# Kernel optimization log

Measured on AMD Instinct MI355X. Metric: run time of the kernel, lower is better.

The kernel has to match this reference:

```python
import jax, jax.numpy as jnp
import numpy as np
from jax import lax

BATCH = 4096
HID = 512
T = 20


def setup_inputs() -> dict:
    key = jax.random.key(0)
    ks = jax.random.split(key, 12)
    B2 = BATCH * 2
    inp = {
        "x": jax.random.normal(ks[0], (BATCH, 2, T, 2), jnp.float32),
        "x_agents": jax.random.normal(ks[1], (BATCH, 2), jnp.float32),  # unused by forward
        "h0": jax.random.normal(ks[2], (B2, HID), jnp.float32),
        "c0": jax.random.normal(ks[3], (B2, HID), jnp.float32),
        # LSTMCell params (PyTorch layout: gates stacked as [i, f, g, o])
        "W_ih": jax.random.normal(ks[4], (4 * HID, 2), jnp.float32) * 0.05,
        "W_hh": jax.random.normal(ks[5], (4 * HID, HID), jnp.float32) * 0.05,
        "b_ih": jax.random.normal(ks[6], (4 * HID,), jnp.float32) * 0.05,
        "b_hh": jax.random.normal(ks[7], (4 * HID,), jnp.float32) * 0.05,
        # MLP head
        "fc1_w": jax.random.normal(ks[8], (HID, 2 * T * HID), jnp.float32) * 0.01,
        "fc1_b": jax.random.normal(ks[9], (HID,), jnp.float32) * 0.01,
        "fc2_w": jax.random.normal(ks[10], (1, HID), jnp.float32) * 0.05,
        "fc2_b": jax.random.normal(ks[11], (1,), jnp.float32) * 0.05,
        "training_step": 2,
    }
    return inp


def reference(x, x_agents, h0, c0, W_ih, W_hh, b_ih, b_hh, fc1_w, fc1_b, fc2_w, fc2_b, training_step):
    # training_step == 2 path (default) of the original module.
    batch = x.shape[0]
    H = W_hh.shape[1]
    xs = x.reshape(batch * 2, T, 2).transpose(1, 0, 2)  # [T, B2, 2]

    def step(carry, xt):
        h, c = carry
        gates = xt @ W_ih.T + b_ih + h @ W_hh.T + b_hh  # [B2, 4H]
        i, f, g, o = jnp.split(gates, 4, axis=-1)
        i = jax.nn.sigmoid(i)
        f = jax.nn.sigmoid(f)
        g = jnp.tanh(g)
        o = jax.nn.sigmoid(o)
        c_new = f * c + i * g
        h_new = o * jnp.tanh(c_new)
        return (h_new, c_new), h_new

    _, hs = lax.scan(step, (h0, c0), xs)  # hs: [T, B2, H]
    states = hs.transpose(1, 0, 2).reshape(batch, 2 * T * H)  # [batch, 2*T*H]
    out = jax.nn.relu(states @ fc1_w.T + fc1_b) @ fc2_w.T + fc2_b
    return jax.nn.sigmoid(out)
```

## Files before the change

kernel.cpp:

```cpp
#include <hip/hip_runtime.h>
#include <hip/hip_bf16.h>

#define TSTEPS 20
#define SMEM_BYTES 131072

typedef __bf16 bf16x8 __attribute__((ext_vector_type(8)));
typedef float f32x4 __attribute__((ext_vector_type(4)));
typedef unsigned short u16;

__device__ __forceinline__ u16 f2bf(float f) {
  unsigned u = __builtin_bit_cast(unsigned, f);
  u = (u + 0x7FFFu + ((u >> 16) & 1u)) >> 16;
  return (u16)u;
}
__device__ __forceinline__ float rcp_(float v) { return __builtin_amdgcn_rcpf(v); }
__device__ __forceinline__ float sig_(float v) { return rcp_(1.f + __expf(-v)); }
__device__ __forceinline__ float tanh_(float v) { return 1.f - 2.f * rcp_(1.f + __expf(2.f * v)); }

#define MFMA16(a, b, c) __builtin_amdgcn_mfma_f32_16x16x32_bf16((a), (b), (c), 0, 0, 0)
#define BAR() asm volatile("s_barrier" ::: "memory")
#define WAITV(n) asm volatile("s_waitcnt vmcnt(" #n ")" ::: "memory")
#define WAITLG() asm volatile("s_waitcnt lgkmcnt(0)" ::: "memory")

__device__ __forceinline__ void gload16(const u16* g, u16* lds) {
#if defined(__HIP_DEVICE_COMPILE__)
  __builtin_amdgcn_global_load_lds(
      (const __attribute__((address_space(1))) unsigned*)g,
      (__attribute__((address_space(3))) unsigned*)lds, 16, 0, 0);
#endif
}

__global__ void convert_f32_bf16(const float* __restrict__ s, u16* __restrict__ d, int n) {
  int i = (blockIdx.x * blockDim.x + threadIdx.x) * 4;
  if (i + 3 < n) {
    float4 v = *reinterpret_cast<const float4*>(s + i);
    ushort4 o;
    o.x = f2bf(v.x); o.y = f2bf(v.y); o.z = f2bf(v.z); o.w = f2bf(v.w);
    *reinterpret_cast<ushort4*>(d + i) = o;
  }
}

__global__ void convert_whh_p(const float* __restrict__ w, u16* __restrict__ d) {
  int p = blockIdx.x;
  int k = threadIdx.x;
  int j = p & 15, f = (p >> 4) & 3, wg = (p >> 6) & 3, s = p >> 8;
  int orig = (f << 9) + (s << 6) + (wg << 4) + j;
  d[p * 512 + k] = f2bf(w[orig * 512 + k]);
}

__global__ void bx_prep(const float* __restrict__ Wih, const float* __restrict__ bih,
                        const float* __restrict__ bhh, u16* __restrict__ Bx) {
  int p = blockIdx.x * blockDim.x + threadIdx.x;
  if (p >= 2048) return;
  int j = p & 15, f = (p >> 4) & 3, wg = (p >> 6) & 3, s = p >> 8;
  int o = (f << 9) + (s << 6) + (wg << 4) + j;
  u16* row = Bx + p * 32;
  row[0] = f2bf(Wih[o * 2 + 0]);
  row[1] = f2bf(Wih[o * 2 + 1]);
  row[2] = f2bf(bih[o] + bhh[o]);
#pragma unroll
  for (int k = 3; k < 32; ++k) row[k] = 0;
}

__global__ void init_state(const float* __restrict__ h0, const float* __restrict__ c0,
                           u16* __restrict__ hbf, float* __restrict__ cws,
                           float* __restrict__ facc, int nh, int nacc) {
  int i = blockIdx.x * blockDim.x + threadIdx.x;
  if (i < nh) {
    hbf[i] = f2bf(h0[i]);
    int r = i & 3, mt = (i >> 2) & 7, lane = (i >> 5) & 63, wid = (i >> 11) & 7, bid = i >> 14;
    int s = (bid >> 3) & 7, nb = (bid & 7) * 4 + (bid >> 6);
    int wm = wid >> 2, wn = wid & 3;
    int jl = lane & 15, kg = lane >> 4;
    int n = nb * 256 + wm * 128 + mt * 16 + kg * 4 + r;
    int u = s * 64 + wn * 16 + jl;
    cws[i] = c0[n * 512 + u];
  }
  if (i < nacc) facc[i] = 0.f;
}

__global__ __launch_bounds__(512, 1) void step256(
    const u16* __restrict__ Wp,
    const u16* __restrict__ Bxg,
    const float* __restrict__ x,
    const u16* __restrict__ hin,
    u16* __restrict__ hout,
    float* __restrict__ cws,
    const u16* __restrict__ fc1w,
    float* __restrict__ facc,
    int t, int doLstm, int doFc1) {
  extern __shared__ char S[];

  const int tid = threadIdx.x;
  const int lane = tid & 63, wid = tid >> 6;
  const int jl = lane & 15, kg = lane >> 4;
  const int bid = blockIdx.x;
  const int s = (bid >> 3) & 7;
  const int nb = (bid & 7) * 4 + (bid >> 6);
  const int n0 = nb * 256;
  const int srow = tid >> 3;
  const int sw = (tid & 7) ^ (srow & 7);

  if (doLstm) {
    const int wm = wid >> 2, wn = wid & 3;
    const int u = s * 64 + wn * 16 + jl;
    const int swz0 = (kg ^ (jl & 7)) * 16;
    const int swz1 = ((4 + kg) ^ (jl & 7)) * 16;
    const int aB0 = wm * 16384 + jl * 128 + swz0;
    const int aB1 = wm * 16384 + jl * 128 + swz1;
    const int bB0 = 32768 + wn * 8192 + jl * 128 + swz0;
    const int bB1 = 32768 + wn * 8192 + jl * 128 + swz1;
    const u16* srcA = hin + (n0 + srow) * 512 + sw * 8;
    const u16* srcB = Wp + (s * 256 + srow) * 512 + sw * 8;

    f32x4 acc[8][4];
#pragma unroll
    for (int mt = 0; mt < 8; ++mt)
#pragma unroll
      for (int f = 0; f < 4; ++f) acc[mt][f] = (f32x4){0.f, 0.f, 0.f, 0.f};

    float2 xv = {0.f, 0.f};
    if (tid < 256) xv = *reinterpret_cast<const float2*>(x + (n0 + tid) * 40 + t * 2);
    {
      const int r0 = tid >> 2, ch = tid & 3;
      gload16(Bxg + (s * 256 + 0 * 128 + r0) * 32 + ch * 8, (u16*)(S + 32768 + 0 * 8192 + wid * 1024));
      gload16(Bxg + (s * 256 + 1 * 128 + r0) * 32 + ch * 8, (u16*)(S + 32768 + 1 * 8192 + wid * 1024));
    }
#pragma unroll
    for (int q = 0; q < 4; ++q) {
      gload16(srcA + q * 32768, (u16*)(S + 65536 + q * 8192 + wid * 1024));
      gload16(srcB + q * 32768, (u16*)(S + 65536 + 32768 + q * 8192 + wid * 1024));
    }
    if (tid < 256) {
      u16 row0[8] = {f2bf(xv.x), f2bf(xv.y), 0x3F80u, 0, 0, 0, 0, 0};
      *reinterpret_cast<uint4*>(S + tid * 64) = *reinterpret_cast<const uint4*>(row0);
      uint4 z = {0u, 0u, 0u, 0u};
      *reinterpret_cast<uint4*>(S + tid * 64 + 16) = z;
      *reinterpret_cast<uint4*>(S + tid * 64 + 32) = z;
      *reinterpret_cast<uint4*>(S + tid * 64 + 48) = z;
    }
    WAITLG();
    WAITV(8);
    BAR();
    {
#pragma unroll
      for (int mt = 0; mt < 8; ++mt) {
        bf16x8 a = *reinterpret_cast<const bf16x8*>(S + (wm * 128 + mt * 16 + jl) * 64 + kg * 16);
#pragma unroll
        for (int f = 0; f < 4; ++f) {
          bf16x8 b = *reinterpret_cast<const bf16x8*>(S + 32768 + (wn * 64 + f * 16 + jl) * 64 + kg * 16);
          acc[mt][f] = MFMA16(a, b, acc[mt][f]);
        }
      }
    }
    BAR();

#define LSTAGE(kt, p)                                                              \
  do {                                                                             \
    _Pragma("unroll") for (int q = 0; q < 4; ++q) {                                \
      gload16(srcA + q * 32768 + (kt) * 64, (u16*)(S + (p) * 65536 + q * 8192 + wid * 1024)); \
      gload16(srcB + q * 32768 + (kt) * 64, (u16*)(S + (p) * 65536 + 32768 + q * 8192 + wid * 1024)); \
    }                                                                              \
  } while (0)
#define LCOMP(p)                                                                   \
  do {                                                                             \
    bf16x8 a0[8], b0[4];                                                           \
    _Pragma("unroll") for (int mt = 0; mt < 8; ++mt)                               \
        a0[mt] = *reinterpret_cast<const bf16x8*>(S + (p) * 65536 + aB0 + mt * 2048); \
    _Pragma("unroll") for (int f = 0; f < 4; ++f)                                  \
        b0[f] = *reinterpret_cast<const bf16x8*>(S + (p) * 65536 + bB0 + f * 2048); \
    _Pragma("unroll") for (int mt = 0; mt < 8; ++mt)                               \
      _Pragma("unroll") for (int f = 0; f < 4; ++f)                                \
        acc[mt][f] = MFMA16(a0[mt], b0[f], acc[mt][f]);                            \
    _Pragma("unroll") for (int mt = 0; mt < 8; ++mt)                               \
        a0[mt] = *reinterpret_cast<const bf16x8*>(S + (p) * 65536 + aB1 + mt * 2048); \
    _Pragma("unroll") for (int f = 0; f < 4; ++f)                                  \
        b0[f] = *reinterpret_cast<const bf16x8*>(S + (p) * 65536 + bB1 + f * 2048); \
    _Pragma("unroll") for (int mt = 0; mt < 8; ++mt)                               \
      _Pragma("unroll") for (int f = 0; f < 4; ++f)                                \
        acc[mt][f] = MFMA16(a0[mt], b0[f], acc[mt][f]);                            \
  } while (0)

#pragma unroll
    for (int kt = 0; kt < 8; ++kt) {
      if (kt < 7) {
        if ((kt + 1) & 1) LSTAGE(kt + 1, 0); else LSTAGE(kt + 1, 1);
        WAITV(8);
      } else {
        WAITV(0);
      }
      BAR();
      if (kt & 1) LCOMP(0); else LCOMP(1);
      BAR();
    }

    float* cbase = cws + ((bid * 8 + wid) * 64 + lane) * 32;
#pragma unroll
    for (int mt = 0; mt < 8; ++mt) {
      f32x4 cv = *reinterpret_cast<f32x4*>(cbase + mt * 4);
      f32x4 cn;
      float hn[4];
#pragma unroll
      for (int r = 0; r < 4; ++r) {
        float iv = sig_(acc[mt][0][r]);
        float fv = sig_(acc[mt][1][r]);
        float gv = tanh_(acc[mt][2][r]);
        float ov = sig_(acc[mt][3][r]);
        float c2 = fv * cv[r] + iv * gv;
        cn[r] = c2;
        hn[r] = ov * tanh_(c2);
      }
      *reinterpret_cast<f32x4*>(cbase + mt * 4) = cn;
#pragma unroll
      for (int r = 0; r < 4; ++r)
        hout[(n0 + wm * 128 + mt * 16 + kg * 4 + r) * 512 + u] = f2bf(hn[r]);
    }
  }

  if (doFc1) {
    const int Fm0 = nb * 128, Fj0 = s * 64;
    const int Fwm = wid >> 1, Fwn = wid & 1;
    const int tf = t - 1;
    const int swz0 = (kg ^ (jl & 7)) * 16;
    const int swz1 = ((4 + kg) ^ (jl & 7)) * 16;
    const int faB0 = Fwm * 4096 + jl * 128 + swz0;
    const int faB1 = Fwm * 4096 + jl * 128 + swz1;
    const int fbB0 = 16384 + Fwn * 4096 + jl * 128 + swz0;
    const int fbB1 = 16384 + Fwn * 4096 + jl * 128 + swz1;
    const u16* fsrcA = hin + 2 * (Fm0 + srow) * 512 + sw * 8;
    const u16* fsrcB = fc1w + (Fj0 + srow) * 20480 + tf * 512 + sw * 8;

    f32x4 fa[2][2];
#pragma unroll
    for (int a = 0; a < 2; ++a)
#pragma unroll
      for (int b = 0; b < 2; ++b) fa[a][b] = (f32x4){0.f, 0.f, 0.f, 0.f};

#define FSTAGE(kt, p)                                                              \
  do {                                                                             \
    const int an_ = (kt) >> 3, kc_ = ((kt) & 7) * 64;                              \
    gload16(fsrcA + 0 * 65536 + an_ * 512 + kc_, (u16*)(S + (p) * 32768 + 0 * 8192 + wid * 1024)); \
    gload16(fsrcA + 1 * 65536 + an_ * 512 + kc_, (u16*)(S + (p) * 32768 + 1 * 8192 + wid * 1024)); \
    gload16(fsrcB + an_ * 10240 + kc_, (u16*)(S + (p) * 32768 + 16384 + wid * 1024)); \
  } while (0)
#define FCOMP(p)                                                                   \
  do {                                                                             \
    bf16x8 af[2], bf[2];                                                           \
    _Pragma("unroll") for (int mf = 0; mf < 2; ++mf)                               \
        af[mf] = *reinterpret_cast<const bf16x8*>(S + (p) * 32768 + faB0 + mf * 2048); \
    _Pragma("unroll") for (int jf = 0; jf < 2; ++jf)                               \
        bf[jf] = *reinterpret_cast<const bf16x8*>(S + (p) * 32768 + fbB0 + jf * 2048); \
    _Pragma("unroll") for (int mf = 0; mf < 2; ++mf)                               \
      _Pragma("unroll") for (int jf = 0; jf < 2; ++jf)                             \
        fa[mf][jf] = MFMA16(af[mf], bf[jf], fa[mf][jf]);                           \
    _Pragma("unroll") for (int mf = 0; mf < 2; ++mf)                               \
        af[mf] = *reinterpret_cast<const bf16x8*>(S + (p) * 32768 + faB1 + mf * 2048); \
    _Pragma("unroll") for (int jf = 0; jf < 2; ++jf)                               \
        bf[jf] = *reinterpret_cast<const bf16x8*>(S + (p) * 32768 + fbB1 + jf * 2048); \
    _Pragma("unroll") for (int mf = 0; mf < 2; ++mf)                               \
      _Pragma("unroll") for (int jf = 0; jf < 2; ++jf)                             \
        fa[mf][jf] = MFMA16(af[mf], bf[jf], fa[mf][jf]);                           \
  } while (0)

    FSTAGE(0, 0);
#pragma unroll
    for (int kt = 0; kt < 16; ++kt) {
      if (kt < 15) {
        if ((kt + 1) & 1) FSTAGE(kt + 1, 1); else FSTAGE(kt + 1, 0);
        WAITV(3);
      } else {
        WAITV(0);
      }
      BAR();
      if (kt & 1) FCOMP(1); else FCOMP(0);
      BAR();
    }
#pragma unroll
    for (int mf = 0; mf < 2; ++mf)
#pragma unroll
      for (int jf = 0; jf < 2; ++jf) {
        int j = Fj0 + Fwn * 32 + jf * 16 + jl;
#pragma unroll
        for (int r = 0; r < 4; ++r) {
          int m = Fm0 + Fwm * 32 + mf * 16 + kg * 4 + r;
          facc[m * 512 + j] += fa[mf][jf][r];
        }
      }
  }
}

__global__ __launch_bounds__(256) void head_kernel(
    const float* __restrict__ acc, const float* __restrict__ fc1b,
    const float* __restrict__ fc2w, const float* __restrict__ fc2b,
    float* __restrict__ out) {
  int lane = threadIdx.x & 63;
  int row = blockIdx.x * 4 + (threadIdx.x >> 6);
  float sum = 0.f;
#pragma unroll
  for (int j = lane; j < 512; j += 64)
    sum += fmaxf(acc[row * 512 + j] + fc1b[j], 0.f) * fc2w[j];
#pragma unroll
  for (int off = 32; off; off >>= 1) sum += __shfl_down(sum, off);
  if (lane == 0) out[row] = sig_(sum + fc2b[0]);
}

extern "C" void kernel_launch(void* const* d_in, const int* in_sizes, int n_in,
                              void* d_out, int out_size, void* d_ws, size_t ws_size,
                              hipStream_t stream) {
  const float* x = (const float*)d_in[0];
  const float* h0 = (const float*)d_in[2];
  const float* c0 = (const float*)d_in[3];
  const float* Wih = (const float*)d_in[4];
  const float* Whh = (const float*)d_in[5];
  const float* bih = (const float*)d_in[6];
  const float* bhh = (const float*)d_in[7];
  const float* fc1w = (const float*)d_in[8];
  const float* fc1b = (const float*)d_in[9];
  const float* fc2w = (const float*)d_in[10];
  const float* fc2b = (const float*)d_in[11];
  float* out = (float*)d_out;

  char* ws = (char*)d_ws;
  const size_t MB = 1 << 20;
  u16* Wp = (u16*)(ws);
  u16* fc1_bf = (u16*)(ws + 2 * MB);
  u16* hbf0 = (u16*)(ws + 22 * MB);
  u16* hbf1 = (u16*)(ws + 30 * MB);
  float* cws = (float*)(ws + 38 * MB);
  float* facc = (float*)(ws + 54 * MB);
  u16* Bxg = (u16*)(ws + 62 * MB);

  (void)hipFuncSetAttribute(reinterpret_cast<const void*>(step256),
                            hipFuncAttributeMaxDynamicSharedMemorySize, SMEM_BYTES);

  convert_whh_p<<<2048, 512, 0, stream>>>(Whh, Wp);
  bx_prep<<<8, 256, 0, stream>>>(Wih, bih, bhh, Bxg);
  convert_f32_bf16<<<10240, 256, 0, stream>>>(fc1w, fc1_bf, 512 * 20480);
  init_state<<<16384, 256, 0, stream>>>(h0, c0, hbf0, cws, facc, 8192 * 512, 4096 * 512);

  u16* hb[2] = {hbf0, hbf1};
  for (int t = 0; t <= TSTEPS; ++t) {
    step256<<<256, 512, SMEM_BYTES, stream>>>(
        Wp, Bxg, x, hb[t & 1], hb[(t + 1) & 1], cws, fc1_bf, facc,
        t, t < TSTEPS ? 1 : 0, t > 0 ? 1 : 0);
  }
  head_kernel<<<1024, 256, 0, stream>>>(facc, fc1b, fc2w, fc2b, out);
}
```

Before: 712.2 us.

## Fuse fc1 accumulation into LSTM K-loop reusing staged h tiles from LDS

The fc1 partial GEMM for the previous timestep now runs inside the LSTM recurrent K-loop. It reads the h tile already staged in LDS instead of loading h and fc1 weights through a separate pipelined phase. fc1 weights are pre-permuted into an MFMA-fragment layout so each lane loads its B operands directly from global memory, and a small fc1_tail kernel handles the final timestep. This removes the second load pipeline and extra barriers per step, at the cost of more register pressure and global loads interleaved with the LSTM MFMAs, plus s_setprio hints.

```diff
diff --git a/kernel.cpp b/kernel.cpp
--- a/kernel.cpp
+++ b/kernel.cpp
@@ -30,22 +30,30 @@
 #endif
 }
 
-__global__ void convert_f32_bf16(const float* __restrict__ s, u16* __restrict__ d, int n) {
-  int i = (blockIdx.x * blockDim.x + threadIdx.x) * 4;
-  if (i + 3 < n) {
-    float4 v = *reinterpret_cast<const float4*>(s + i);
-    ushort4 o;
-    o.x = f2bf(v.x); o.y = f2bf(v.y); o.z = f2bf(v.z); o.w = f2bf(v.w);
-    *reinterpret_cast<ushort4*>(d + i) = o;
-  }
-}
-
 __global__ void convert_whh_p(const float* __restrict__ w, u16* __restrict__ d) {
   int p = blockIdx.x;
   int k = threadIdx.x;
   int j = p & 15, f = (p >> 4) & 3, wg = (p >> 6) & 3, s = p >> 8;
   int orig = (f << 9) + (s << 6) + (wg << 4) + j;
   d[p * 512 + k] = f2bf(w[orig * 512 + k]);
+}
+
+__global__ void fc1p_prep(const float* __restrict__ w, u16* __restrict__ d) {
+  int id = blockIdx.x * blockDim.x + threadIdx.x;
+  int jl = id & 15, t1 = id >> 4;
+  int kg = t1 & 3, t2 = t1 >> 2;
+  int jf = t2 & 1, t3 = t2 >> 1;
+  int Fwn = t3 & 1, t4 = t3 >> 1;
+  int kk2 = t4 & 31, t5 = t4 >> 5;
+  int tf = t5 % 20, s = t5 / 20;
+  int j = s * 64 + Fwn * 32 + jf * 16 + jl;
+  int k = kk2 * 32 + kg * 8;
+  const float* src = w + j * 20480 + (k >> 9) * 10240 + tf * 512 + (k & 511);
+  float4 v0 = *reinterpret_cast<const float4*>(src);
+  float4 v1 = *reinterpret_cast<const float4*>(src + 4);
+  u16* dst = d + id * 8;
+  dst[0] = f2bf(v0.x); dst[1] = f2bf(v0.y); dst[2] = f2bf(v0.z); dst[3] = f2bf(v0.w);
+  dst[4] = f2bf(v1.x); dst[5] = f2bf(v1.y); dst[6] = f2bf(v1.z); dst[7] = f2bf(v1.w);
 }
 
 __global__ void bx_prep(const float* __restrict__ Wih, const float* __restrict__ bih,
@@ -86,9 +94,9 @@
     const u16* __restrict__ hin,
     u16* __restrict__ hout,
     float* __restrict__ cws,
-    const u16* __restrict__ fc1w,
+    const u16* __restrict__ fc1p,
     float* __restrict__ facc,
-    int t, int doLstm, int doFc1) {
+    int t, int doFacc) {
   extern __shared__ char S[];
 
   const int tid = threadIdx.x;
@@ -101,59 +109,66 @@
   const int srow = tid >> 3;
   const int sw = (tid & 7) ^ (srow & 7);
 
-  if (doLstm) {
-    const int wm = wid >> 2, wn = wid & 3;
-    const int u = s * 64 + wn * 16 + jl;
-    const int swz0 = (kg ^ (jl & 7)) * 16;
-    const int swz1 = ((4 + kg) ^ (jl & 7)) * 16;
-    const int aB0 = wm * 16384 + jl * 128 + swz0;
-    const int aB1 = wm * 16384 + jl * 128 + swz1;
-    const int bB0 = 32768 + wn * 8192 + jl * 128 + swz0;
-    const int bB1 = 32768 + wn * 8192 + jl * 128 + swz1;
-    const u16* srcA = hin + (n0 + srow) * 512 + sw * 8;
-    const u16* srcB = Wp + (s * 256 + srow) * 512 + sw * 8;
-
-    f32x4 acc[8][4];
-#pragma unroll
-    for (int mt = 0; mt < 8; ++mt)
-#pragma unroll
-      for (int f = 0; f < 4; ++f) acc[mt][f] = (f32x4){0.f, 0.f, 0.f, 0.f};
-
-    float2 xv = {0.f, 0.f};
-    if (tid < 256) xv = *reinterpret_cast<const float2*>(x + (n0 + tid) * 40 + t * 2);
-    {
-      const int r0 = tid >> 2, ch = tid & 3;
-      gload16(Bxg + (s * 256 + 0 * 128 + r0) * 32 + ch * 8, (u16*)(S + 32768 + 0 * 8192 + wid * 1024));
-      gload16(Bxg + (s * 256 + 1 * 128 + r0) * 32 + ch * 8, (u16*)(S + 32768 + 1 * 8192 + wid * 1024));
-    }
-#pragma unroll
-    for (int q = 0; q < 4; ++q) {
-      gload16(srcA + q * 32768, (u16*)(S + 65536 + q * 8192 + wid * 1024));
-      gload16(srcB + q * 32768, (u16*)(S + 65536 + 32768 + q * 8192 + wid * 1024));
-    }
-    if (tid < 256) {
-      u16 row0[8] = {f2bf(xv.x), f2bf(xv.y), 0x3F80u, 0, 0, 0, 0, 0};
-      *reinterpret_cast<uint4*>(S + tid * 64) = *reinterpret_cast<const uint4*>(row0);
-      uint4 z = {0u, 0u, 0u, 0u};
-      *reinterpret_cast<uint4*>(S + tid * 64 + 16) = z;
-      *reinterpret_cast<uint4*>(S + tid * 64 + 32) = z;
-      *reinterpret_cast<uint4*>(S + tid * 64 + 48) = z;
-    }
-    WAITLG();
-    WAITV(8);
-    BAR();
-    {
-#pragma unroll
-      for (int mt = 0; mt < 8; ++mt) {
-        bf16x8 a = *reinterpret_cast<const bf16x8*>(S + (wm * 128 + mt * 16 + jl) * 64 + kg * 16);
-#pragma unroll
-        for (int f = 0; f < 4; ++f) {
-          bf16x8 b = *reinterpret_cast<const bf16x8*>(S + 32768 + (wn * 64 + f * 16 + jl) * 64 + kg * 16);
-          acc[mt][f] = MFMA16(a, b, acc[mt][f]);
-        }
-      }
-    }
-    BAR();
+  const int wm = wid >> 2, wn = wid & 3;
+  const int Fwm = wid >> 1, Fwn = wid & 1;
+  const int u = s * 64 + wn * 16 + jl;
+  const int tf = (t > 0) ? (t - 1) : 0;
+  const int swz0 = (kg ^ (jl & 7)) * 16;
+  const int swz1 = ((4 + kg) ^ (jl & 7)) * 16;
+  const int aB0 = wm * 16384 + jl * 128 + swz0;
+  const int aB1 = wm * 16384 + jl * 128 + swz1;
+  const int bB0 = 32768 + wn * 8192 + jl * 128 + swz0;
+  const int bB1 = 32768 + wn * 8192 + jl * 128 + swz1;
+  const u16* srcA = hin + (n0 + srow) * 512 + sw * 8;
+  const u16* srcB = Wp + (s * 256 + srow) * 512 + sw * 8;
+  const u16* fbl = fc1p + (s * 20 + tf) * 65536 + Fwn * 1024 + kg * 128 + jl * 8;
+
+  f32x4 acc[8][4];
+#pragma unroll
+  for (int mt = 0; mt < 8; ++mt)
+#pragma unroll
+    for (int f = 0; f < 4; ++f) acc[mt][f] = (f32x4){0.f, 0.f, 0.f, 0.f};
+  f32x4 fa[2][2];
+#pragma unroll
+  for (int a = 0; a < 2; ++a)
+#pragma unroll
+    for (int b = 0; b < 2; ++b) fa[a][b] = (f32x4){0.f, 0.f, 0.f, 0.f};
+
+  float2 xv = {0.f, 0.f};
+  if (tid < 256) xv = *reinterpret_cast<const float2*>(x + (n0 + tid) * 40 + t * 2);
+  {
+    const int r0 = tid >> 2, ch = tid & 3;
+    gload16(Bxg + (s * 256 + 0 * 128 + r0) * 32 + ch * 8, (u16*)(S + 32768 + 0 * 8192 + wid * 1024));
+    gload16(Bxg + (s * 256 + 1 * 128 + r0) * 32 + ch * 8, (u16*)(S + 32768 + 1 * 8192 + wid * 1024));
+  }
+#pragma unroll
+  for (int q = 0; q < 4; ++q) {
+    gload16(srcA + q * 32768, (u16*)(S + 65536 + q * 8192 + wid * 1024));
+    gload16(srcB + q * 32768, (u16*)(S + 65536 + 32768 + q * 8192 + wid * 1024));
+  }
+  if (tid < 256) {
+    u16 row0[8] = {f2bf(xv.x), f2bf(xv.y), 0x3F80u, 0, 0, 0, 0, 0};
+    *reinterpret_cast<uint4*>(S + tid * 64) = *reinterpret_cast<const uint4*>(row0);
+    uint4 z = {0u, 0u, 0u, 0u};
+    *reinterpret_cast<uint4*>(S + tid * 64 + 16) = z;
+    *reinterpret_cast<uint4*>(S + tid * 64 + 32) = z;
+    *reinterpret_cast<uint4*>(S + tid * 64 + 48) = z;
+  }
+  WAITLG();
+  WAITV(8);
+  BAR();
+  {
+#pragma unroll
+    for (int mt = 0; mt < 8; ++mt) {
+      bf16x8 a = *reinterpret_cast<const bf16x8*>(S + (wm * 128 + mt * 16 + jl) * 64 + kg * 16);
+#pragma unroll
+      for (int f = 0; f < 4; ++f) {
+        bf16x8 b = *reinterpret_cast<const bf16x8*>(S + 32768 + (wn * 64 + f * 16 + jl) * 64 + kg * 16);
+        acc[mt][f] = MFMA16(a, b, acc[mt][f]);
+      }
+    }
+  }
+  BAR();
 
 #define LSTAGE(kt, p)                                                              \
   do {                                                                             \
@@ -182,99 +197,71 @@
   } while (0)
 
 #pragma unroll
-    for (int kt = 0; kt < 8; ++kt) {
-      if (kt < 7) {
-        if ((kt + 1) & 1) LSTAGE(kt + 1, 0); else LSTAGE(kt + 1, 1);
-        WAITV(8);
-      } else {
-        WAITV(0);
-      }
-      BAR();
-      if (kt & 1) LCOMP(0); else LCOMP(1);
-      BAR();
-    }
-
-    float* cbase = cws + ((bid * 8 + wid) * 64 + lane) * 32;
-#pragma unroll
-    for (int mt = 0; mt < 8; ++mt) {
-      f32x4 cv = *reinterpret_cast<f32x4*>(cbase + mt * 4);
-      f32x4 cn;
-      float hn[4];
-#pragma unroll
-      for (int r = 0; r < 4; ++r) {
-        float iv = sig_(acc[mt][0][r]);
-        float fv = sig_(acc[mt][1][r]);
-        float gv = tanh_(acc[mt][2][r]);
-        float ov = sig_(acc[mt][3][r]);
-        float c2 = fv * cv[r] + iv * gv;
-        cn[r] = c2;
-        hn[r] = ov * tanh_(c2);
-      }
-      *reinterpret_cast<f32x4*>(cbase + mt * 4) = cn;
-#pragma unroll
-      for (int r = 0; r < 4; ++r)
-        hout[(n0 + wm * 128 + mt * 16 + kg * 4 + r) * 512 + u] = f2bf(hn[r]);
-    }
-  }
-
-  if (doFc1) {
+  for (int kt = 0; kt < 8; ++kt) {
+    bf16x8 fbe[2][2], fbo[2][2];
+#pragma unroll
+    for (int jf = 0; jf < 2; ++jf)
+#pragma unroll
+      for (int kk = 0; kk < 2; ++kk) {
+        fbe[jf][kk] = *reinterpret_cast<const bf16x8*>(fbl + (2 * kt + kk) * 2048 + jf * 512);
+        fbo[jf][kk] = *reinterpret_cast<const bf16x8*>(fbl + (2 * kt + 16 + kk) * 2048 + jf * 512);
+      }
+    if (kt < 7) {
+      if ((kt + 1) & 1) LSTAGE(kt + 1, 0); else LSTAGE(kt + 1, 1);
+      WAITV(16);
+    } else {
+      WAITV(8);
+    }
+    BAR();
+    __builtin_amdgcn_s_setprio(1);
+    if (kt & 1) LCOMP(0); else LCOMP(1);
+    __builtin_amdgcn_s_setprio(0);
+    {
+      const int P = (kt & 1) ? 0 : 1;
+#pragma unroll
+      for (int kk = 0; kk < 2; ++kk) {
+#pragma unroll
+        for (int mf = 0; mf < 2; ++mf) {
+          const int er = Fwm * 64 + mf * 32 + 2 * jl;
+          bf16x8 ae = *reinterpret_cast<const bf16x8*>(
+              S + P * 65536 + er * 128 + (((kk * 4) + kg) ^ (er & 7)) * 16);
+          bf16x8 ao = *reinterpret_cast<const bf16x8*>(
+              S + P * 65536 + (er + 1) * 128 + (((kk * 4) + kg) ^ ((er + 1) & 7)) * 16);
+#pragma unroll
+          for (int jf = 0; jf < 2; ++jf) {
+            fa[mf][jf] = MFMA16(ae, fbe[jf][kk], fa[mf][jf]);
+            fa[mf][jf] = MFMA16(ao, fbo[jf][kk], fa[mf][jf]);
+          }
+        }
+      }
+    }
+    BAR();
+  }
+
+  float* cbase = cws + ((bid * 8 + wid) * 64 + lane) * 32;
+#pragma unroll
+  for (int mt = 0; mt < 8; ++mt) {
+    f32x4 cv = *reinterpret_cast<f32x4*>(cbase + mt * 4);
+    f32x4 cn;
+    float hn[4];
+#pragma unroll
+    for (int r = 0; r < 4; ++r) {
+      float iv = sig_(acc[mt][0][r]);
+      float fv = sig_(acc[mt][1][r]);
+      float gv = tanh_(acc[mt][2][r]);
+      float ov = sig_(acc[mt][3][r]);
+      float c2 = fv * cv[r] + iv * gv;
+      cn[r] = c2;
+      hn[r] = ov * tanh_(c2);
+    }
+    *reinterpret_cast<f32x4*>(cbase + mt * 4) = cn;
+#pragma unroll
+    for (int r = 0; r < 4; ++r)
+      hout[(n0 + wm * 128 + mt * 16 + kg * 4 + r) * 512 + u] = f2bf(hn[r]);
+  }
+
+  if (doFacc) {
     const int Fm0 = nb * 128, Fj0 = s * 64;
-    const int Fwm = wid >> 1, Fwn = wid & 1;
-    const int tf = t - 1;
-    const int swz0 = (kg ^ (jl & 7)) * 16;
-    const int swz1 = ((4 + kg) ^ (jl & 7)) * 16;
-    const int faB0 = Fwm * 4096 + jl * 128 + swz0;
-    const int faB1 = Fwm * 4096 + jl * 128 + swz1;
-    const int fbB0 = 16384 + Fwn * 4096 + jl * 128 + swz0;
-    const int fbB1 = 16384 + Fwn * 4096 + jl * 128 + swz1;
-    const u16* fsrcA = hin + 2 * (Fm0 + srow) * 512 + sw * 8;
-    const u16* fsrcB = fc1w + (Fj0 + srow) * 20480 + tf * 512 + sw * 8;
-
-    f32x4 fa[2][2];
-#pragma unroll
-    for (int a = 0; a < 2; ++a)
-#pragma unroll
-      for (int b = 0; b < 2; ++b) fa[a][b] = (f32x4){0.f, 0.f, 0.f, 0.f};
-
-#define FSTAGE(kt, p)                                                              \
-  do {                                                                             \
-    const int an_ = (kt) >> 3, kc_ = ((kt) & 7) * 64;                              \
-    gload16(fsrcA + 0 * 65536 + an_ * 512 + kc_, (u16*)(S + (p) * 32768 + 0 * 8192 + wid * 1024)); \
-    gload16(fsrcA + 1 * 65536 + an_ * 512 + kc_, (u16*)(S + (p) * 32768 + 1 * 8192 + wid * 1024)); \
-    gload16(fsrcB + an_ * 10240 + kc_, (u16*)(S + (p) * 32768 + 16384 + wid * 1024)); \
-  } while (0)
-#define FCOMP(p)                                                                   \
-  do {                                                                             \
-    bf16x8 af[2], bf[2];                                                           \
-    _Pragma("unroll") for (int mf = 0; mf < 2; ++mf)                               \
-        af[mf] = *reinterpret_cast<const bf16x8*>(S + (p) * 32768 + faB0 + mf * 2048); \
-    _Pragma("unroll") for (int jf = 0; jf < 2; ++jf)                               \
-        bf[jf] = *reinterpret_cast<const bf16x8*>(S + (p) * 32768 + fbB0 + jf * 2048); \
-    _Pragma("unroll") for (int mf = 0; mf < 2; ++mf)                               \
-      _Pragma("unroll") for (int jf = 0; jf < 2; ++jf)                             \
-        fa[mf][jf] = MFMA16(af[mf], bf[jf], fa[mf][jf]);                           \
-    _Pragma("unroll") for (int mf = 0; mf < 2; ++mf)                               \
-        af[mf] = *reinterpret_cast<const bf16x8*>(S + (p) * 32768 + faB1 + mf * 2048); \
-    _Pragma("unroll") for (int jf = 0; jf < 2; ++jf)                               \
-        bf[jf] = *reinterpret_cast<const bf16x8*>(S + (p) * 32768 + fbB1 + jf * 2048); \
-    _Pragma("unroll") for (int mf = 0; mf < 2; ++mf)                               \
-      _Pragma("unroll") for (int jf = 0; jf < 2; ++jf)                             \
-        fa[mf][jf] = MFMA16(af[mf], bf[jf], fa[mf][jf]);                           \
-  } while (0)
-
-    FSTAGE(0, 0);
-#pragma unroll
-    for (int kt = 0; kt < 16; ++kt) {
-      if (kt < 15) {
-        if ((kt + 1) & 1) FSTAGE(kt + 1, 1); else FSTAGE(kt + 1, 0);
-        WAITV(3);
-      } else {
-        WAITV(0);
-      }
-      BAR();
-      if (kt & 1) FCOMP(1); else FCOMP(0);
-      BAR();
-    }
 #pragma unroll
     for (int mf = 0; mf < 2; ++mf)
 #pragma unroll
@@ -287,6 +274,89 @@
         }
       }
   }
+}
+
+__global__ __launch_bounds__(512, 1) void fc1_tail(
+    const u16* __restrict__ hin, const u16* __restrict__ fc1p,
+    float* __restrict__ facc) {
+  extern __shared__ char S[];
+  const int tid = threadIdx.x;
+  const int lane = tid & 63, wid = tid >> 6;
+  const int jl = lane & 15, kg = lane >> 4;
+  const int bid = blockIdx.x;
+  const int s = (bid >> 3) & 7;
+  const int nb = (bid & 7) * 4 + (bid >> 6);
+  const int n0 = nb * 256;
+  const int srow = tid >> 3;
+  const int sw = (tid & 7) ^ (srow & 7);
+  const int Fwm = wid >> 1, Fwn = wid & 1;
+  const u16* srcA = hin + (n0 + srow) * 512 + sw * 8;
+  const u16* fbl = fc1p + (s * 20 + 19) * 65536 + Fwn * 1024 + kg * 128 + jl * 8;
+
+  f32x4 fa[2][2];
+#pragma unroll
+  for (int a = 0; a < 2; ++a)
+#pragma unroll
+    for (int b = 0; b < 2; ++b) fa[a][b] = (f32x4){0.f, 0.f, 0.f, 0.f};
+
+#pragma unroll
+  for (int q = 0; q < 4; ++q)
+    gload16(srcA + q * 32768, (u16*)(S + 65536 + q * 8192 + wid * 1024));
+
+#pragma unroll
+  for (int kt = 0; kt < 8; ++kt) {
+    bf16x8 fbe[2][2], fbo[2][2];
+#pragma unroll
+    for (int jf = 0; jf < 2; ++jf)
+#pragma unroll
+      for (int kk = 0; kk < 2; ++kk) {
+        fbe[jf][kk] = *reinterpret_cast<const bf16x8*>(fbl + (2 * kt + kk) * 2048 + jf * 512);
+        fbo[jf][kk] = *reinterpret_cast<const bf16x8*>(fbl + (2 * kt + 16 + kk) * 2048 + jf * 512);
+      }
+    if (kt < 7) {
+      const int pn = ((kt + 1) & 1) ? 0 : 1;
+#pragma unroll
+      for (int q = 0; q < 4; ++q)
+        gload16(srcA + q * 32768 + (kt + 1) * 64, (u16*)(S + pn * 65536 + q * 8192 + wid * 1024));
+      WAITV(12);
+    } else {
+      WAITV(8);
+    }
+    BAR();
+    {
+      const int P = (kt & 1) ? 0 : 1;
+#pragma unroll
+      for (int kk = 0; kk < 2; ++kk) {
+#pragma unroll
+        for (int mf = 0; mf < 2; ++mf) {
+          const int er = Fwm * 64 + mf * 32 + 2 * jl;
+          bf16x8 ae = *reinterpret_cast<const bf16x8*>(
+              S + P * 65536 + er * 128 + (((kk * 4) + kg) ^ (er & 7)) * 16);
+          bf16x8 ao = *reinterpret_cast<const bf16x8*>(
+              S + P * 65536 + (er + 1) * 128 + (((kk * 4) + kg) ^ ((er + 1) & 7)) * 16);
+#pragma unroll
+          for (int jf = 0; jf < 2; ++jf) {
+            fa[mf][jf] = MFMA16(ae, fbe[jf][kk], fa[mf][jf]);
+            fa[mf][jf] = MFMA16(ao, fbo[jf][kk], fa[mf][jf]);
+          }
+        }
+      }
+    }
+    BAR();
+  }
+
+  const int Fm0 = nb * 128, Fj0 = s * 64;
+#pragma unroll
+  for (int mf = 0; mf < 2; ++mf)
+#pragma unroll
+    for (int jf = 0; jf < 2; ++jf) {
+      int j = Fj0 + Fwn * 32 + jf * 16 + jl;
+#pragma unroll
+      for (int r = 0; r < 4; ++r) {
+        int m = Fm0 + Fwm * 32 + mf * 16 + kg * 4 + r;
+        facc[m * 512 + j] += fa[mf][jf][r];
+      }
+    }
 }
 
 __global__ __launch_bounds__(256) void head_kernel(
@@ -323,7 +393,7 @@
   char* ws = (char*)d_ws;
   const size_t MB = 1 << 20;
   u16* Wp = (u16*)(ws);
-  u16* fc1_bf = (u16*)(ws + 2 * MB);
+  u16* fc1p = (u16*)(ws + 2 * MB);
   u16* hbf0 = (u16*)(ws + 22 * MB);
   u16* hbf1 = (u16*)(ws + 30 * MB);
   float* cws = (float*)(ws + 38 * MB);
@@ -332,17 +402,19 @@
 
   (void)hipFuncSetAttribute(reinterpret_cast<const void*>(step256),
                             hipFuncAttributeMaxDynamicSharedMemorySize, SMEM_BYTES);
+  (void)hipFuncSetAttribute(reinterpret_cast<const void*>(fc1_tail),
+                            hipFuncAttributeMaxDynamicSharedMemorySize, SMEM_BYTES);
 
   convert_whh_p<<<2048, 512, 0, stream>>>(Whh, Wp);
   bx_prep<<<8, 256, 0, stream>>>(Wih, bih, bhh, Bxg);
-  convert_f32_bf16<<<10240, 256, 0, stream>>>(fc1w, fc1_bf, 512 * 20480);
+  fc1p_prep<<<2560, 512, 0, stream>>>(fc1w, fc1p);
   init_state<<<16384, 256, 0, stream>>>(h0, c0, hbf0, cws, facc, 8192 * 512, 4096 * 512);
 
   u16* hb[2] = {hbf0, hbf1};
-  for (int t = 0; t <= TSTEPS; ++t) {
+  for (int t = 0; t < TSTEPS; ++t) {
     step256<<<256, 512, SMEM_BYTES, stream>>>(
-        Wp, Bxg, x, hb[t & 1], hb[(t + 1) & 1], cws, fc1_bf, facc,
-        t, t < TSTEPS ? 1 : 0, t > 0 ? 1 : 0);
-  }
+        Wp, Bxg, x, hb[t & 1], hb[(t + 1) & 1], cws, fc1p, facc, t, t > 0 ? 1 : 0);
+  }
+  fc1_tail<<<256, 512, SMEM_BYTES, stream>>>(hb[0], fc1p, facc);
   head_kernel<<<1024, 256, 0, stream>>>(facc, fc1b, fc2w, fc2b, out);
 }
```

Result: slower. 780.0 us (+9.5%).

## Store LSTM cell state in fp16 and double FC1 staging tile per barrier

Applied to the files above, without the earlier changes.

The cell state buffer is switched from fp32 to fp16, which halves the global read and write traffic for c on every timestep. The FC1 partial-GEMM pipeline now stages 128-wide K chunks (two 64-wide halves) per stage, using 64KB buffers. That halves the number of barrier-separated iterations, from 16 to 8. The head sigmoid now uses an exact divide, and the workspace offsets are compacted; the trade-off is reduced cell-state precision accumulated across 20 steps.

```diff
diff --git a/kernel.cpp b/kernel.cpp
--- a/kernel.cpp
+++ b/kernel.cpp
@@ -6,6 +6,7 @@
 
 typedef __bf16 bf16x8 __attribute__((ext_vector_type(8)));
 typedef float f32x4 __attribute__((ext_vector_type(4)));
+typedef _Float16 f16x4 __attribute__((ext_vector_type(4)));
 typedef unsigned short u16;
 
 __device__ __forceinline__ u16 f2bf(float f) {
@@ -63,7 +64,7 @@
 }
 
 __global__ void init_state(const float* __restrict__ h0, const float* __restrict__ c0,
-                           u16* __restrict__ hbf, float* __restrict__ cws,
+                           u16* __restrict__ hbf, _Float16* __restrict__ cws,
                            float* __restrict__ facc, int nh, int nacc) {
   int i = blockIdx.x * blockDim.x + threadIdx.x;
   if (i < nh) {
@@ -74,7 +75,7 @@
     int jl = lane & 15, kg = lane >> 4;
     int n = nb * 256 + wm * 128 + mt * 16 + kg * 4 + r;
     int u = s * 64 + wn * 16 + jl;
-    cws[i] = c0[n * 512 + u];
+    cws[i] = (_Float16)c0[n * 512 + u];
   }
   if (i < nacc) facc[i] = 0.f;
 }
@@ -85,7 +86,7 @@
     const float* __restrict__ x,
     const u16* __restrict__ hin,
     u16* __restrict__ hout,
-    float* __restrict__ cws,
+    _Float16* __restrict__ cws,
     const u16* __restrict__ fc1w,
     float* __restrict__ facc,
     int t, int doLstm, int doFc1) {
@@ -194,11 +195,11 @@
       BAR();
     }
 
-    float* cbase = cws + ((bid * 8 + wid) * 64 + lane) * 32;
+    _Float16* cbase = cws + ((bid * 8 + wid) * 64 + lane) * 32;
 #pragma unroll
     for (int mt = 0; mt < 8; ++mt) {
-      f32x4 cv = *reinterpret_cast<f32x4*>(cbase + mt * 4);
-      f32x4 cn;
+      f16x4 cv = *reinterpret_cast<f16x4*>(cbase + mt * 4);
+      f16x4 cn;
       float hn[4];
 #pragma unroll
       for (int r = 0; r < 4; ++r) {
@@ -206,11 +207,11 @@
         float fv = sig_(acc[mt][1][r]);
         float gv = tanh_(acc[mt][2][r]);
         float ov = sig_(acc[mt][3][r]);
-        float c2 = fv * cv[r] + iv * gv;
-        cn[r] = c2;
+        float c2 = fv * (float)cv[r] + iv * gv;
+        cn[r] = (_Float16)c2;
         hn[r] = ov * tanh_(c2);
       }
-      *reinterpret_cast<f32x4*>(cbase + mt * 4) = cn;
+      *reinterpret_cast<f16x4*>(cbase + mt * 4) = cn;
 #pragma unroll
       for (int r = 0; r < 4; ++r)
         hout[(n0 + wm * 128 + mt * 16 + kg * 4 + r) * 512 + u] = f2bf(hn[r]);
@@ -221,14 +222,6 @@
     const int Fm0 = nb * 128, Fj0 = s * 64;
     const int Fwm = wid >> 1, Fwn = wid & 1;
     const int tf = t - 1;
-    const int swz0 = (kg ^ (jl & 7)) * 16;
-    const int swz1 = ((4 + kg) ^ (jl & 7)) * 16;
-    const int faB0 = Fwm * 4096 + jl * 128 + swz0;
-    const int faB1 = Fwm * 4096 + jl * 128 + swz1;
-    const int fbB0 = 16384 + Fwn * 4096 + jl * 128 + swz0;
-    const int fbB1 = 16384 + Fwn * 4096 + jl * 128 + swz1;
-    const u16* fsrcA = hin + 2 * (Fm0 + srow) * 512 + sw * 8;
-    const u16* fsrcB = fc1w + (Fj0 + srow) * 20480 + tf * 512 + sw * 8;
 
     f32x4 fa[2][2];
 #pragma unroll
@@ -238,41 +231,44 @@
 
 #define FSTAGE(kt, p)                                                              \
   do {                                                                             \
-    const int an_ = (kt) >> 3, kc_ = ((kt) & 7) * 64;                              \
-    gload16(fsrcA + 0 * 65536 + an_ * 512 + kc_, (u16*)(S + (p) * 32768 + 0 * 8192 + wid * 1024)); \
-    gload16(fsrcA + 1 * 65536 + an_ * 512 + kc_, (u16*)(S + (p) * 32768 + 1 * 8192 + wid * 1024)); \
-    gload16(fsrcB + an_ * 10240 + kc_, (u16*)(S + (p) * 32768 + 16384 + wid * 1024)); \
+    const int an_ = (kt) >> 2, hb_ = ((kt) & 3) * 128;                             \
+    _Pragma("unroll") for (int kh = 0; kh < 2; ++kh) {                             \
+      _Pragma("unroll") for (int q = 0; q < 2; ++q)                                \
+        gload16(hin + (2 * (Fm0 + q * 64 + srow) + an_) * 512 + hb_ + kh * 64 + sw * 8, \
+                (u16*)(S + (p) * 65536 + kh * 16384 + q * 8192 + wid * 1024));     \
+      gload16(fc1w + (Fj0 + srow) * 20480 + an_ * 10240 + tf * 512 + hb_ + kh * 64 + sw * 8, \
+              (u16*)(S + (p) * 65536 + 32768 + kh * 8192 + wid * 1024));           \
+    }                                                                              \
   } while (0)
 #define FCOMP(p)                                                                   \
   do {                                                                             \
-    bf16x8 af[2], bf[2];                                                           \
-    _Pragma("unroll") for (int mf = 0; mf < 2; ++mf)                               \
-        af[mf] = *reinterpret_cast<const bf16x8*>(S + (p) * 32768 + faB0 + mf * 2048); \
-    _Pragma("unroll") for (int jf = 0; jf < 2; ++jf)                               \
-        bf[jf] = *reinterpret_cast<const bf16x8*>(S + (p) * 32768 + fbB0 + jf * 2048); \
-    _Pragma("unroll") for (int mf = 0; mf < 2; ++mf)                               \
+    _Pragma("unroll") for (int kk = 0; kk < 4; ++kk) {                             \
+      const int kh_ = kk >> 1;                                                     \
+      const int cs_ = (((kk & 1) * 4 + kg) ^ (jl & 7)) * 16;                       \
+      bf16x8 af[2], bf[2];                                                         \
+      _Pragma("unroll") for (int mf = 0; mf < 2; ++mf)                             \
+          af[mf] = *reinterpret_cast<const bf16x8*>(                               \
+              S + (p) * 65536 + kh_ * 16384 + (Fwm * 32 + mf * 16 + jl) * 128 + cs_); \
       _Pragma("unroll") for (int jf = 0; jf < 2; ++jf)                             \
-        fa[mf][jf] = MFMA16(af[mf], bf[jf], fa[mf][jf]);                           \
-    _Pragma("unroll") for (int mf = 0; mf < 2; ++mf)                               \
-        af[mf] = *reinterpret_cast<const bf16x8*>(S + (p) * 32768 + faB1 + mf * 2048); \
-    _Pragma("unroll") for (int jf = 0; jf < 2; ++jf)                               \
-        bf[jf] = *reinterpret_cast<const bf16x8*>(S + (p) * 32768 + fbB1 + jf * 2048); \
-    _Pragma("unroll") for (int mf = 0; mf < 2; ++mf)                               \
-      _Pragma("unroll") for (int jf = 0; jf < 2; ++jf)                             \
-        fa[mf][jf] = MFMA16(af[mf], bf[jf], fa[mf][jf]);                           \
+          bf[jf] = *reinterpret_cast<const bf16x8*>(                               \
+              S + (p) * 65536 + 32768 + kh_ * 8192 + (Fwn * 32 + jf * 16 + jl) * 128 + cs_); \
+      _Pragma("unroll") for (int mf = 0; mf < 2; ++mf)                             \
+        _Pragma("unroll") for (int jf = 0; jf < 2; ++jf)                           \
+          fa[mf][jf] = MFMA16(af[mf], bf[jf], fa[mf][jf]);                         \
+    }                                                                              \
   } while (0)
 
-    FSTAGE(0, 0);
-#pragma unroll
-    for (int kt = 0; kt < 16; ++kt) {
-      if (kt < 15) {
-        if ((kt + 1) & 1) FSTAGE(kt + 1, 1); else FSTAGE(kt + 1, 0);
-        WAITV(3);
+    FSTAGE(0, 1);
+#pragma unroll
+    for (int kt = 0; kt < 8; ++kt) {
+      if (kt < 7) {
+        if ((kt + 1) & 1) FSTAGE(kt + 1, 0); else FSTAGE(kt + 1, 1);
+        WAITV(6);
       } else {
         WAITV(0);
       }
       BAR();
-      if (kt & 1) FCOMP(1); else FCOMP(0);
+      if (kt & 1) FCOMP(0); else FCOMP(1);
       BAR();
     }
 #pragma unroll
@@ -301,7 +297,7 @@
     sum += fmaxf(acc[row * 512 + j] + fc1b[j], 0.f) * fc2w[j];
 #pragma unroll
   for (int off = 32; off; off >>= 1) sum += __shfl_down(sum, off);
-  if (lane == 0) out[row] = sig_(sum + fc2b[0]);
+  if (lane == 0) out[row] = 1.f / (1.f + __expf(-(sum + fc2b[0])));
 }
 
 extern "C" void kernel_launch(void* const* d_in, const int* in_sizes, int n_in,
@@ -326,9 +322,9 @@
   u16* fc1_bf = (u16*)(ws + 2 * MB);
   u16* hbf0 = (u16*)(ws + 22 * MB);
   u16* hbf1 = (u16*)(ws + 30 * MB);
-  float* cws = (float*)(ws + 38 * MB);
-  float* facc = (float*)(ws + 54 * MB);
-  u16* Bxg = (u16*)(ws + 62 * MB);
+  _Float16* cws = (_Float16*)(ws + 38 * MB);
+  float* facc = (float*)(ws + 46 * MB);
+  u16* Bxg = (u16*)(ws + 54 * MB);
 
   (void)hipFuncSetAttribute(reinterpret_cast<const void*>(step256),
                             hipFuncAttributeMaxDynamicSharedMemorySize, SMEM_BYTES);
```

Result: faster. 611.1 us (-14.2%).
